# Kernel tuning notes

Hardware: AMD Instinct MI355X
Metric: run time of the kernel (lower is better)

The kernel has to match this reference:

```python
import jax, jax.numpy as jnp
import numpy as np

T, H, I, E, TOP_K = 4096, 2048, 768, 16, 2


def _pack_i2s(tern):
    # tern: int8 in {-1,0,1}, shape [..., K] with K % 4 == 0
    m = (tern + 1).astype(jnp.uint8)  # map to {0,1,2}
    m = m.reshape(*tern.shape[:-1], -1, 4)
    return (m[..., 0] | (m[..., 1] << 2) | (m[..., 2] << 4) | (m[..., 3] << 6)).astype(jnp.uint8)


def _quantize_alpha(alpha):
    # per-column alpha -> int8 with global scale (quantize_alpha_int8)
    scale = jnp.maximum(jnp.abs(alpha).max(), 1e-8) / 127.0
    q = jnp.clip(jnp.round(alpha / scale), -128, 127).astype(jnp.int8)
    return q, scale.astype(jnp.float32)


def _unpack_i2s(packed, K, alpha):
    # packed: uint8 [..., N, K//4]; alpha: [..., K] per input column
    shifts = jnp.array([0, 2, 4, 6], dtype=jnp.uint8)
    ext = (packed[..., None] >> shifts) & jnp.uint8(3)  # [..., N, K//4, 4]
    vals = ext.reshape(*packed.shape[:-1], K).astype(jnp.float32) - 1.0  # {-1,0,1}
    return vals * alpha[..., None, :]


def setup_inputs() -> dict:
    key = jax.random.key(0)
    ks = jax.random.split(key, 6)
    x = jax.random.normal(ks[0], (T, H), dtype=jnp.float32)
    router_logits = jax.random.normal(ks[1], (T, E), dtype=jnp.float32)
    tern13 = jax.random.randint(ks[2], (E, 2 * I, H), -1, 2, dtype=jnp.int8)
    tern2 = jax.random.randint(ks[3], (E, H, I), -1, 2, dtype=jnp.int8)
    a13 = jax.random.uniform(ks[4], (E, H), minval=0.01, maxval=0.05, dtype=jnp.float32)
    a2 = jax.random.uniform(ks[5], (E, I), minval=0.01, maxval=0.05, dtype=jnp.float32)
    w13_alpha_q, w13_alpha_scale = _quantize_alpha(a13)
    w2_alpha_q, w2_alpha_scale = _quantize_alpha(a2)
    return {
        "x": x,
        "router_logits": router_logits,
        "w13_packed": _pack_i2s(tern13),
        "w13_alpha_q": w13_alpha_q,
        "w13_alpha_scale": w13_alpha_scale,
        "w2_packed": _pack_i2s(tern2),
        "w2_alpha_q": w2_alpha_q,
        "w2_alpha_scale": w2_alpha_scale,
    }


def reference(x, router_logits, w13_packed, w13_alpha_q, w13_alpha_scale,
              w2_packed, w2_alpha_q, w2_alpha_scale):
    # dequant int8 alphas, then dequant 2-bit ternary weights
    a13 = w13_alpha_q.astype(jnp.float32) * w13_alpha_scale  # [E, H]
    a2 = w2_alpha_q.astype(jnp.float32) * w2_alpha_scale     # [E, I]
    w13 = _unpack_i2s(w13_packed, H, a13)  # [E, 2I, H]
    w2 = _unpack_i2s(w2_packed, I, a2)     # [E, H, I]

    # top-k routing with renormalized softmax weights
    probs = jax.nn.softmax(router_logits, axis=-1)
    topw, topi = jax.lax.top_k(probs, TOP_K)           # [T, k]
    topw = topw / topw.sum(axis=-1, keepdims=True)
    combine = jnp.sum(jax.nn.one_hot(topi, E, dtype=x.dtype) * topw[..., None], axis=1)  # [T, E]

    # grouped expert matmuls (dense dispatch over experts)
    gu = jnp.einsum('th,enh->ten', x, w13)             # [T, E, 2I]
    gate, up = jnp.split(gu, 2, axis=-1)
    act = jax.nn.silu(gate) * up                       # [T, E, I]
    down = jnp.einsum('tei,ehi->teh', act, w2)         # [T, E, H]
    return jnp.einsum('te,teh->th', combine, down)     # [T, H]
```

## Files before the change

### kernel.cpp

```cpp
#include <hip/hip_runtime.h>
#include <stdint.h>

#define T_TOK 4096
#define HDIM  2048
#define IDIM  768
#define NEXP  16
#define NPAIR (T_TOK * 2)
#define PAIR_CAP_FB (NPAIR + 128)
#define PAIR_CAP    (NPAIR + 256)

typedef float f32x4 __attribute__((ext_vector_type(4)));
typedef __bf16 bf16x8 __attribute__((ext_vector_type(8)));
typedef unsigned short u16x8 __attribute__((ext_vector_type(8)));
typedef unsigned int u32;
typedef const __attribute__((address_space(1))) u32* as1_u32p;
typedef __attribute__((address_space(3))) u32* as3_u32p;

__device__ __forceinline__ unsigned short f2bf(float f) {
  u32 u = __float_as_uint(f);
  u += 0x7FFFu + ((u >> 16) & 1u);
  return (unsigned short)(u >> 16);
}

__device__ __forceinline__ unsigned short tb(int m) {
  return m == 0 ? (unsigned short)0xBF80 : (m == 2 ? (unsigned short)0x3F80 : (unsigned short)0);
}

__device__ __forceinline__ f32x4 mfma16(bf16x8 a, bf16x8 b, f32x4 c) {
  return __builtin_amdgcn_mfma_f32_16x16x32_bf16(a, b, c, 0, 0, 0);
}

__global__ __launch_bounds__(256) void route_kernel(
    const float* __restrict__ logits, int* __restrict__ counts,
    int* __restrict__ t2i, float* __restrict__ t2w) {
  const int t = blockIdx.x * 256 + threadIdx.x;
  if (t >= T_TOK) return;
  const float* l = logits + t * NEXP;
  float m0 = -1e30f, m1 = -1e30f;
  int i0 = 0, i1 = 0;
#pragma unroll
  for (int j = 0; j < NEXP; ++j) {
    const float v = l[j];
    if (v > m0) { m1 = m0; i1 = i0; m0 = v; i0 = j; }
    else if (v > m1) { m1 = v; i1 = j; }
  }
  const float w0 = 1.0f / (1.0f + expf(m1 - m0));
  t2i[t] = i0 | (i1 << 8);
  t2w[t] = w0;
  atomicAdd(&counts[i0], 1);
  atomicAdd(&counts[i1], 1);
}

__global__ void scan_kernel(const int* __restrict__ counts,
                            int* __restrict__ offs, int* __restrict__ cursor) {
  if (threadIdx.x == 0) {
    int s = 0;
    for (int e = 0; e < NEXP; ++e) { offs[e] = s; cursor[e] = s; s += counts[e]; }
    offs[NEXP] = s;
  }
}

__global__ __launch_bounds__(256) void fill_kernel(
    const int* __restrict__ t2i, const float* __restrict__ t2w,
    int* __restrict__ cursor, int* __restrict__ pair_token,
    float* __restrict__ pair_wt, int* __restrict__ pair_eid) {
  const int t = blockIdx.x * 256 + threadIdx.x;
  if (t >= T_TOK) return;
  const int ii = t2i[t];
  const float w0 = t2w[t];
  const int i0 = ii & 255, i1 = (ii >> 8) & 255;
  const int p0 = atomicAdd(&cursor[i0], 1);
  pair_token[p0] = t; pair_wt[p0] = w0; pair_eid[p0] = i0;
  const int p1 = atomicAdd(&cursor[i1], 1);
  pair_token[p1] = t; pair_wt[p1] = 1.0f - w0; pair_eid[p1] = i1;
}

__global__ __launch_bounds__(256) void xg_kernel(
    const float* __restrict__ x, const int* __restrict__ a13q,
    const float* __restrict__ s13p, const int* __restrict__ pair_token,
    const int* __restrict__ pair_eid, unsigned short* __restrict__ xg) {
  const int p = blockIdx.x;
  const int t = pair_token[p];
  const int e = pair_eid[p];
  const float s13 = *s13p;
  const int h0 = threadIdx.x * 8;
  const float* xp = x + (size_t)t * HDIM + h0;
  const int* ap = a13q + (size_t)e * HDIM + h0;
  const float4 x0 = ((const float4*)xp)[0];
  const float4 x1 = ((const float4*)xp)[1];
  const int4 a0 = ((const int4*)ap)[0];
  const int4 a1 = ((const int4*)ap)[1];
  u16x8 q;
  q[0] = f2bf(x0.x * (float)a0.x * s13);
  q[1] = f2bf(x0.y * (float)a0.y * s13);
  q[2] = f2bf(x0.z * (float)a0.z * s13);
  q[3] = f2bf(x0.w * (float)a0.w * s13);
  q[4] = f2bf(x1.x * (float)a1.x * s13);
  q[5] = f2bf(x1.y * (float)a1.y * s13);
  q[6] = f2bf(x1.z * (float)a1.z * s13);
  q[7] = f2bf(x1.w * (float)a1.w * s13);
  *(u16x8*)(xg + (size_t)p * HDIM + h0) = q;
}

__global__ __launch_bounds__(256, 2) void gemm1_kernel(
    const int* __restrict__ w13p, const int* __restrict__ a2q,
    const float* __restrict__ s2p, const int* __restrict__ counts,
    const int* __restrict__ offs, const unsigned short* __restrict__ xg,
    unsigned short* __restrict__ act) {
  const int nT = blockIdx.x;
  const int mT = blockIdx.y;
  const int e  = blockIdx.z;
  const int cnt = counts[e];
  if (mT * 256 >= cnt) return;
  const int base = offs[e];
  const int tid = threadIdx.x;

  __shared__ unsigned short sA[256 * 32];
  __shared__ unsigned short sB[128 * 40];
  __shared__ uint2 lut[256];

  {
    const int b = tid;
    const u32 lo = (u32)tb(b & 3) | ((u32)tb((b >> 2) & 3) << 16);
    const u32 hi = (u32)tb((b >> 4) & 3) | ((u32)tb((b >> 6) & 3) << 16);
    lut[b] = make_uint2(lo, hi);
  }
  __syncthreads();

  const int wave = tid >> 6, lane = tid & 63;
  const int quad = lane >> 4, ln = lane & 15;

  const int bn = tid >> 1, bhalf = tid & 1;
  const int grow = (bn < 64) ? (nT * 64 + bn) : (IDIM + nT * 64 + (bn - 64));
  const int* bptr = w13p + ((size_t)e * (2 * IDIM) + grow) * (HDIM / 4) + bhalf * 4;
  unsigned short* sBw = sB + bn * 40 + (bhalf << 4);

  const int arow = lane >> 2;
  const int acol = (lane & 3) * 8;
  const size_t arow0 = (size_t)(base + mT * 256);

  f32x4 acc[4][8] = {};

  for (int kt = 0; kt < HDIM / 32; ++kt) {
#pragma unroll
    for (int c = 0; c < 4; ++c) {
      const unsigned short* gp =
          xg + (arow0 + c * 64 + wave * 16 + arow) * HDIM + kt * 32 + acol;
      unsigned short* lp = sA + (c * 64 + wave * 16) * 32;
      __builtin_amdgcn_global_load_lds((as1_u32p)(const void*)gp, (as3_u32p)(void*)lp, 16, 0, 0);
    }
    {
      const int4 wv = *(const int4*)(bptr + kt * 8);
      const uint2 q0 = lut[wv.x], q1 = lut[wv.y], q2 = lut[wv.z], q3 = lut[wv.w];
      *(uint2*)(sBw + 0) = q0;
      *(uint2*)(sBw + 4) = q1;
      *(uint2*)(sBw + 8) = q2;
      *(uint2*)(sBw + 12) = q3;
    }
    __syncthreads();
    bf16x8 af[4];
#pragma unroll
    for (int mi = 0; mi < 4; ++mi)
      af[mi] = *(const bf16x8*)(sA + (wave * 64 + mi * 16 + ln) * 32 + quad * 8);
#pragma unroll
    for (int ni = 0; ni < 8; ++ni) {
      const bf16x8 bf = *(const bf16x8*)(sB + (ni * 16 + ln) * 40 + quad * 8);
#pragma unroll
      for (int mi = 0; mi < 4; ++mi) acc[mi][ni] = mfma16(af[mi], bf, acc[mi][ni]);
    }
    __syncthreads();
  }

  const float s2 = *s2p;
#pragma unroll
  for (int ni = 0; ni < 4; ++ni) {
    const int i = nT * 64 + ni * 16 + ln;
    const float a2v = (float)a2q[e * IDIM + i] * s2;
#pragma unroll
    for (int mi = 0; mi < 4; ++mi) {
      const f32x4 g = acc[mi][ni];
      const f32x4 u = acc[mi][ni + 4];
#pragma unroll
      for (int r = 0; r < 4; ++r) {
        const int m = mT * 256 + wave * 64 + mi * 16 + quad * 4 + r;
        if (m < cnt) {
          const float gv = g[r];
          const float av = gv / (1.0f + __expf(-gv)) * u[r];
          act[(size_t)(base + m) * IDIM + i] = f2bf(av * a2v);
        }
      }
    }
  }
}

__global__ __launch_bounds__(256, 2) void gemm2_kernel(
    const int* __restrict__ w2p, const int* __restrict__ counts,
    const int* __restrict__ offs, const int* __restrict__ pair_token,
    const float* __restrict__ pair_wt, const unsigned short* __restrict__ act,
    float* __restrict__ out) {
  const int nT = blockIdx.x;
  const int mT = blockIdx.y;
  const int e  = blockIdx.z;
  const int cnt = counts[e];
  if (mT * 256 >= cnt) return;
  const int base = offs[e];
  const int tid = threadIdx.x;

  __shared__ unsigned short sA[256 * 32];
  __shared__ unsigned short sB[128 * 40];
  __shared__ uint2 lut[256];
  __shared__ int stok[256];
  __shared__ float swt[256];

  {
    const int b = tid;
    const u32 lo = (u32)tb(b & 3) | ((u32)tb((b >> 2) & 3) << 16);
    const u32 hi = (u32)tb((b >> 4) & 3) | ((u32)tb((b >> 6) & 3) << 16);
    lut[b] = make_uint2(lo, hi);
    const int m = mT * 256 + tid;
    const bool v = m < cnt;
    stok[tid] = v ? pair_token[base + m] : 0;
    swt[tid]  = v ? pair_wt[base + m] : 0.0f;
  }
  __syncthreads();

  const int wave = tid >> 6, lane = tid & 63;
  const int quad = lane >> 4, ln = lane & 15;

  const int bn = tid >> 1, bhalf = tid & 1;
  const int* bptr = w2p + ((size_t)e * HDIM + nT * 128 + bn) * (IDIM / 4) + bhalf * 4;
  unsigned short* sBw = sB + bn * 40 + (bhalf << 4);

  const int arow = lane >> 2;
  const int acol = (lane & 3) * 8;
  const size_t arow0 = (size_t)(base + mT * 256);

  f32x4 acc[4][8] = {};

  for (int kt = 0; kt < IDIM / 32; ++kt) {
#pragma unroll
    for (int c = 0; c < 4; ++c) {
      const unsigned short* gp =
          act + (arow0 + c * 64 + wave * 16 + arow) * IDIM + kt * 32 + acol;
      unsigned short* lp = sA + (c * 64 + wave * 16) * 32;
      __builtin_amdgcn_global_load_lds((as1_u32p)(const void*)gp, (as3_u32p)(void*)lp, 16, 0, 0);
    }
    {
      const int4 wv = *(const int4*)(bptr + kt * 8);
      const uint2 q0 = lut[wv.x], q1 = lut[wv.y], q2 = lut[wv.z], q3 = lut[wv.w];
      *(uint2*)(sBw + 0) = q0;
      *(uint2*)(sBw + 4) = q1;
      *(uint2*)(sBw + 8) = q2;
      *(uint2*)(sBw + 12) = q3;
    }
    __syncthreads();
    bf16x8 af[4];
#pragma unroll
    for (int mi = 0; mi < 4; ++mi)
      af[mi] = *(const bf16x8*)(sA + (wave * 64 + mi * 16 + ln) * 32 + quad * 8);
#pragma unroll
    for (int ni = 0; ni < 8; ++ni) {
      const bf16x8 bf = *(const bf16x8*)(sB + (ni * 16 + ln) * 40 + quad * 8);
#pragma unroll
      for (int mi = 0; mi < 4; ++mi) acc[mi][ni] = mfma16(af[mi], bf, acc[mi][ni]);
    }
    __syncthreads();
  }

#pragma unroll
  for (int mi = 0; mi < 4; ++mi) {
#pragma unroll
    for (int r = 0; r < 4; ++r) {
      const int ml = wave * 64 + mi * 16 + quad * 4 + r;
      const int m = mT * 256 + ml;
      if (m < cnt) {
        const float wgt = swt[ml];
        float* orow = out + (size_t)stok[ml] * HDIM + nT * 128;
#pragma unroll
        for (int ni = 0; ni < 8; ++ni)
          atomicAdd(orow + ni * 16 + ln, wgt * acc[mi][ni][r]);
      }
    }
  }
}

__global__ __launch_bounds__(256) void gemm1_fb(
    const float* __restrict__ x, const int* __restrict__ w13p,
    const int* __restrict__ a13q, const float* __restrict__ s13p,
    const int* __restrict__ a2q, const float* __restrict__ s2p,
    const int* __restrict__ counts, const int* __restrict__ offs,
    const int* __restrict__ pair_token, unsigned short* __restrict__ act) {
  const int nT = blockIdx.x;
  const int mT = blockIdx.y;
  const int e  = blockIdx.z;
  const int cnt = counts[e];
  if (mT * 128 >= cnt) return;
  const int base = offs[e];
  const int tid = threadIdx.x;

  __shared__ float ald[HDIM];
  __shared__ unsigned short sA[128 * 40];
  __shared__ unsigned short sB[128 * 40];
  __shared__ int stok[128];

  const float s13 = *s13p;
  for (int h = tid; h < HDIM; h += 256) ald[h] = (float)a13q[e * HDIM + h] * s13;
  if (tid < 128) {
    const int m = mT * 128 + tid;
    stok[tid] = (m < cnt) ? pair_token[base + m] : 0;
  }
  __syncthreads();

  const int wave = tid >> 6, lane = tid & 63;
  const int quad = lane >> 4, ln = lane & 15;

  const int ar = tid >> 1, akh = (tid & 1) << 4;
  const size_t xrow = (size_t)stok[ar] * HDIM;
  const int bn = tid >> 1, bhalf = tid & 1;
  const int grow = (bn < 64) ? (nT * 64 + bn) : (IDIM + nT * 64 + (bn - 64));
  const int* bptr = w13p + ((size_t)e * (2 * IDIM) + grow) * (HDIM / 4) + bhalf * 4;
  unsigned short* sAw = sA + ar * 40 + akh;
  unsigned short* sBw = sB + bn * 40 + (bhalf << 4);

  f32x4 acc[2][8] = {};

  for (int kt = 0; kt < HDIM / 32; ++kt) {
    const int k0 = kt * 32;
    {
      const float* xp = x + xrow + k0 + akh;
      const float* ap = ald + k0 + akh;
      const float4 f0 = ((const float4*)xp)[0];
      const float4 f1 = ((const float4*)xp)[1];
      const float4 f2 = ((const float4*)xp)[2];
      const float4 f3 = ((const float4*)xp)[3];
      u16x8 q0, q1;
      q0[0] = f2bf(f0.x * ap[0]);  q0[1] = f2bf(f0.y * ap[1]);
      q0[2] = f2bf(f0.z * ap[2]);  q0[3] = f2bf(f0.w * ap[3]);
      q0[4] = f2bf(f1.x * ap[4]);  q0[5] = f2bf(f1.y * ap[5]);
      q0[6] = f2bf(f1.z * ap[6]);  q0[7] = f2bf(f1.w * ap[7]);
      q1[0] = f2bf(f2.x * ap[8]);  q1[1] = f2bf(f2.y * ap[9]);
      q1[2] = f2bf(f2.z * ap[10]); q1[3] = f2bf(f2.w * ap[11]);
      q1[4] = f2bf(f3.x * ap[12]); q1[5] = f2bf(f3.y * ap[13]);
      q1[6] = f2bf(f3.z * ap[14]); q1[7] = f2bf(f3.w * ap[15]);
      *(u16x8*)(sAw) = q0;
      *(u16x8*)(sAw + 8) = q1;
    }
    {
      const int4 wv = *(const int4*)(bptr + kt * 8);
      u16x8 q0, q1;
      q0[0] = tb(wv.x & 3); q0[1] = tb((wv.x >> 2) & 3); q0[2] = tb((wv.x >> 4) & 3); q0[3] = tb((wv.x >> 6) & 3);
      q0[4] = tb(wv.y & 3); q0[5] = tb((wv.y >> 2) & 3); q0[6] = tb((wv.y >> 4) & 3); q0[7] = tb((wv.y >> 6) & 3);
      q1[0] = tb(wv.z & 3); q1[1] = tb((wv.z >> 2) & 3); q1[2] = tb((wv.z >> 4) & 3); q1[3] = tb((wv.z >> 6) & 3);
      q1[4] = tb(wv.w & 3); q1[5] = tb((wv.w >> 2) & 3); q1[6] = tb((wv.w >> 4) & 3); q1[7] = tb((wv.w >> 6) & 3);
      *(u16x8*)(sBw) = q0;
      *(u16x8*)(sBw + 8) = q1;
    }
    __syncthreads();
    bf16x8 af[2];
#pragma unroll
    for (int mi = 0; mi < 2; ++mi)
      af[mi] = *(const bf16x8*)(sA + (wave * 32 + mi * 16 + ln) * 40 + quad * 8);
#pragma unroll
    for (int ni = 0; ni < 8; ++ni) {
      const bf16x8 bf = *(const bf16x8*)(sB + (ni * 16 + ln) * 40 + quad * 8);
      acc[0][ni] = mfma16(af[0], bf, acc[0][ni]);
      acc[1][ni] = mfma16(af[1], bf, acc[1][ni]);
    }
    __syncthreads();
  }

  const float s2 = *s2p;
#pragma unroll
  for (int ni = 0; ni < 4; ++ni) {
    const int i = nT * 64 + ni * 16 + ln;
    const float a2v = (float)a2q[e * IDIM + i] * s2;
#pragma unroll
    for (int mi = 0; mi < 2; ++mi) {
      const f32x4 g = acc[mi][ni];
      const f32x4 u = acc[mi][ni + 4];
#pragma unroll
      for (int r = 0; r < 4; ++r) {
        const int m = mT * 128 + wave * 32 + mi * 16 + quad * 4 + r;
        if (m < cnt) {
          const float gv = g[r];
          const float av = gv / (1.0f + __expf(-gv)) * u[r];
          act[(size_t)(base + m) * IDIM + i] = f2bf(av * a2v);
        }
      }
    }
  }
}

__global__ __launch_bounds__(256) void gemm2_fb(
    const int* __restrict__ w2p, const int* __restrict__ counts,
    const int* __restrict__ offs, const int* __restrict__ pair_token,
    const float* __restrict__ pair_wt, const unsigned short* __restrict__ act,
    float* __restrict__ out) {
  const int nT = blockIdx.x;
  const int mT = blockIdx.y;
  const int e  = blockIdx.z;
  const int cnt = counts[e];
  if (mT * 128 >= cnt) return;
  const int base = offs[e];
  const int tid = threadIdx.x;

  __shared__ unsigned short sA[128 * 32];
  __shared__ unsigned short sB[128 * 40];
  __shared__ int stok[128];
  __shared__ float swt[128];

  if (tid < 128) {
    const int m = mT * 128 + tid;
    const bool v = m < cnt;
    stok[tid] = v ? pair_token[base + m] : 0;
    swt[tid]  = v ? pair_wt[base + m] : 0.0f;
  }

  const int wave = tid >> 6, lane = tid & 63;
  const int quad = lane >> 4, ln = lane & 15;

  const int bn = tid >> 1, bhalf = tid & 1;
  const int* bptr = w2p + ((size_t)e * HDIM + nT * 128 + bn) * (IDIM / 4) + bhalf * 4;
  unsigned short* sBw = sB + bn * 40 + (bhalf << 4);

  const int arow = lane >> 2;
  const int acol8 = (lane & 3) * 8;
  const size_t arow0 = (size_t)(base + mT * 128);

  f32x4 acc[2][8] = {};

  for (int kt = 0; kt < IDIM / 32; ++kt) {
#pragma unroll
    for (int c = 0; c < 2; ++c) {
      const int r = c * 64 + wave * 16 + arow;
      const unsigned short* gp = act + (arow0 + r) * IDIM + kt * 32 + acol8;
      unsigned short* lp = sA + (c * 64 + wave * 16) * 32;
      __builtin_amdgcn_global_load_lds((as1_u32p)(const void*)gp, (as3_u32p)(void*)lp, 16, 0, 0);
    }
    {
      const int4 wv = *(const int4*)(bptr + kt * 8);
      u16x8 q0, q1;
      q0[0] = tb(wv.x & 3); q0[1] = tb((wv.x >> 2) & 3); q0[2] = tb((wv.x >> 4) & 3); q0[3] = tb((wv.x >> 6) & 3);
      q0[4] = tb(wv.y & 3); q0[5] = tb((wv.y >> 2) & 3); q0[6] = tb((wv.y >> 4) & 3); q0[7] = tb((wv.y >> 6) & 3);
      q1[0] = tb(wv.z & 3); q1[1] = tb((wv.z >> 2) & 3); q1[2] = tb((wv.z >> 4) & 3); q1[3] = tb((wv.z >> 6) & 3);
      q1[4] = tb(wv.w & 3); q1[5] = tb((wv.w >> 2) & 3); q1[6] = tb((wv.w >> 4) & 3); q1[7] = tb((wv.w >> 6) & 3);
      *(u16x8*)(sBw) = q0;
      *(u16x8*)(sBw + 8) = q1;
    }
    __syncthreads();
    bf16x8 af[2];
#pragma unroll
    for (int mi = 0; mi < 2; ++mi)
      af[mi] = *(const bf16x8*)(sA + (wave * 32 + mi * 16 + ln) * 32 + quad * 8);
#pragma unroll
    for (int ni = 0; ni < 8; ++ni) {
      const bf16x8 bf = *(const bf16x8*)(sB + (ni * 16 + ln) * 40 + quad * 8);
      acc[0][ni] = mfma16(af[0], bf, acc[0][ni]);
      acc[1][ni] = mfma16(af[1], bf, acc[1][ni]);
    }
    __syncthreads();
  }

#pragma unroll
  for (int mi = 0; mi < 2; ++mi) {
#pragma unroll
    for (int r = 0; r < 4; ++r) {
      const int ml = wave * 32 + mi * 16 + quad * 4 + r;
      const int m = mT * 128 + ml;
      if (m < cnt) {
        const float wgt = swt[ml];
        float* orow = out + (size_t)stok[ml] * HDIM + nT * 128;
#pragma unroll
        for (int ni = 0; ni < 8; ++ni)
          atomicAdd(orow + ni * 16 + ln, wgt * acc[mi][ni][r]);
      }
    }
  }
}

extern "C" void kernel_launch(void* const* d_in, const int* in_sizes, int n_in,
                              void* d_out, int out_size, void* d_ws, size_t ws_size,
                              hipStream_t stream) {
  const float* x      = (const float*)d_in[0];
  const float* logits = (const float*)d_in[1];
  const int*   w13p   = (const int*)d_in[2];
  const int*   a13q   = (const int*)d_in[3];
  const float* s13    = (const float*)d_in[4];
  const int*   w2p    = (const int*)d_in[5];
  const int*   a2q    = (const int*)d_in[6];
  const float* s2     = (const float*)d_in[7];
  float* out = (float*)d_out;

  char* ws = (char*)d_ws;
  int*   counts     = (int*)(ws + 0);
  int*   cursor     = (int*)(ws + 64);
  int*   offs       = (int*)(ws + 128);
  int*   t2i        = (int*)(ws + 256);
  float* t2w        = (float*)(ws + 256 + 4 * T_TOK);
  int*   pair_token = (int*)(ws + 256 + 8 * T_TOK);
  float* pair_wt    = (float*)(ws + 256 + 8 * T_TOK + 4 * PAIR_CAP);
  int*   pair_eid   = (int*)(ws + 256 + 8 * T_TOK + 8 * PAIR_CAP);
  const size_t hdr_end = ((size_t)(256 + 8 * T_TOK + 12 * PAIR_CAP) + 255) & ~(size_t)255;

  const size_t xg_bytes  = (size_t)PAIR_CAP * HDIM * 2;
  const size_t act_bytes = (size_t)PAIR_CAP * IDIM * 2;
  const size_t need_new = hdr_end + xg_bytes + act_bytes;

  hipMemsetAsync(counts, 0, 256, stream);
  hipMemsetAsync(out, 0, (size_t)out_size * sizeof(float), stream);

  route_kernel<<<T_TOK / 256, 256, 0, stream>>>(logits, counts, t2i, t2w);
  scan_kernel<<<1, 64, 0, stream>>>(counts, offs, cursor);
  fill_kernel<<<T_TOK / 256, 256, 0, stream>>>(t2i, t2w, cursor, pair_token, pair_wt, pair_eid);

  if (ws_size >= need_new) {
    unsigned short* xg  = (unsigned short*)(ws + hdr_end);
    unsigned short* act = (unsigned short*)(ws + hdr_end + xg_bytes);
    xg_kernel<<<NPAIR, 256, 0, stream>>>(x, a13q, s13, pair_token, pair_eid, xg);
    gemm1_kernel<<<dim3(12, 16, 16), 256, 0, stream>>>(w13p, a2q, s2, counts, offs, xg, act);
    gemm2_kernel<<<dim3(16, 16, 16), 256, 0, stream>>>(w2p, counts, offs, pair_token,
                                                       pair_wt, act, out);
  } else {
    unsigned short* act = (unsigned short*)(ws + hdr_end);
    gemm1_fb<<<dim3(12, 32, 16), 256, 0, stream>>>(x, w13p, a13q, s13, a2q, s2,
                                                   counts, offs, pair_token, act);
    gemm2_fb<<<dim3(16, 32, 16), 256, 0, stream>>>(w2p, counts, offs, pair_token,
                                                   pair_wt, act, out);
  }
}
```

Measured before the change: 395.3 us.

## Repack ternary weights compactly, shrink GEMM M-tile, replace atomics with combine kernel

Packed ternary weights are stored one byte per int32, so a repack kernel runs each call and compresses them into dense u32 words, cutting the weight bytes the GEMMs read by four. The main GEMMs switch to 128-row M tiles at higher occupancy. gemm2 now writes per-pair outputs to a scratch buffer and a separate combine kernel does the weighted top-2 sum, removing float atomics and the output memset. The cost is extra repack passes on every call, a large fp32 scratch buffer and more kernel launches.

```diff
diff --git a/kernel.cpp b/kernel.cpp
--- a/kernel.cpp
+++ b/kernel.cpp
@@ -6,8 +6,7 @@
 #define IDIM  768
 #define NEXP  16
 #define NPAIR (T_TOK * 2)
-#define PAIR_CAP_FB (NPAIR + 128)
-#define PAIR_CAP    (NPAIR + 256)
+#define PAIR_CAP (NPAIR + 256)
 
 typedef float f32x4 __attribute__((ext_vector_type(4)));
 typedef __bf16 bf16x8 __attribute__((ext_vector_type(8)));
@@ -63,7 +62,8 @@
 __global__ __launch_bounds__(256) void fill_kernel(
     const int* __restrict__ t2i, const float* __restrict__ t2w,
     int* __restrict__ cursor, int* __restrict__ pair_token,
-    float* __restrict__ pair_wt, int* __restrict__ pair_eid) {
+    float* __restrict__ pair_wt, int* __restrict__ pair_eid,
+    int* __restrict__ t2p0, int* __restrict__ t2p1) {
   const int t = blockIdx.x * 256 + threadIdx.x;
   if (t >= T_TOK) return;
   const int ii = t2i[t];
@@ -73,6 +73,21 @@
   pair_token[p0] = t; pair_wt[p0] = w0; pair_eid[p0] = i0;
   const int p1 = atomicAdd(&cursor[i1], 1);
   pair_token[p1] = t; pair_wt[p1] = 1.0f - w0; pair_eid[p1] = i1;
+  t2p0[t] = p0; t2p1[t] = p1;
+}
+
+__global__ __launch_bounds__(256) void repack_kernel(
+    const int* __restrict__ w, u32* __restrict__ o) {
+  const int j0 = (blockIdx.x * 256 + threadIdx.x) * 4;
+  const int4* w4 = (const int4*)w;
+  uint4 r;
+#pragma unroll
+  for (int k = 0; k < 4; ++k) {
+    const int4 a = w4[j0 + k];
+    ((u32*)&r)[k] = (u32)(a.x & 255) | ((u32)(a.y & 255) << 8) |
+                    ((u32)(a.z & 255) << 16) | ((u32)(a.w & 255) << 24);
+  }
+  ((uint4*)o)[blockIdx.x * 256 + threadIdx.x] = r;
 }
 
 __global__ __launch_bounds__(256) void xg_kernel(
@@ -102,8 +117,8 @@
   *(u16x8*)(xg + (size_t)p * HDIM + h0) = q;
 }
 
-__global__ __launch_bounds__(256, 2) void gemm1_kernel(
-    const int* __restrict__ w13p, const int* __restrict__ a2q,
+__global__ __launch_bounds__(256, 3) void gemm1_kernel(
+    const u32* __restrict__ wq13, const int* __restrict__ a2q,
     const float* __restrict__ s2p, const int* __restrict__ counts,
     const int* __restrict__ offs, const unsigned short* __restrict__ xg,
     unsigned short* __restrict__ act) {
@@ -111,11 +126,11 @@
   const int mT = blockIdx.y;
   const int e  = blockIdx.z;
   const int cnt = counts[e];
-  if (mT * 256 >= cnt) return;
+  if (mT * 128 >= cnt) return;
   const int base = offs[e];
   const int tid = threadIdx.x;
 
-  __shared__ unsigned short sA[256 * 32];
+  __shared__ unsigned short sA[128 * 32];
   __shared__ unsigned short sB[128 * 40];
   __shared__ uint2 lut[256];
 
@@ -132,15 +147,218 @@
 
   const int bn = tid >> 1, bhalf = tid & 1;
   const int grow = (bn < 64) ? (nT * 64 + bn) : (IDIM + nT * 64 + (bn - 64));
+  const u32* bptr = wq13 + ((size_t)e * (2 * IDIM) + grow) * (HDIM / 16) + bhalf;
+  unsigned short* sBw = sB + bn * 40 + (bhalf << 4);
+
+  const int arow = lane >> 2;
+  const int acol = (lane & 3) * 8;
+  const size_t arow0 = (size_t)(base + mT * 128);
+
+  f32x4 acc[2][8] = {};
+
+  for (int kt = 0; kt < HDIM / 32; ++kt) {
+#pragma unroll
+    for (int c = 0; c < 2; ++c) {
+      const unsigned short* gp =
+          xg + (arow0 + c * 64 + wave * 16 + arow) * HDIM + kt * 32 + acol;
+      unsigned short* lp = sA + (c * 64 + wave * 16) * 32;
+      __builtin_amdgcn_global_load_lds((as1_u32p)(const void*)gp, (as3_u32p)(void*)lp, 16, 0, 0);
+    }
+    {
+      const u32 wb = bptr[kt * 2];
+      const uint2 q0 = lut[wb & 255], q1 = lut[(wb >> 8) & 255];
+      const uint2 q2 = lut[(wb >> 16) & 255], q3 = lut[wb >> 24];
+      *(uint2*)(sBw + 0) = q0;
+      *(uint2*)(sBw + 4) = q1;
+      *(uint2*)(sBw + 8) = q2;
+      *(uint2*)(sBw + 12) = q3;
+    }
+    __syncthreads();
+    bf16x8 af[2];
+#pragma unroll
+    for (int mi = 0; mi < 2; ++mi)
+      af[mi] = *(const bf16x8*)(sA + (wave * 32 + mi * 16 + ln) * 32 + quad * 8);
+#pragma unroll
+    for (int ni = 0; ni < 8; ++ni) {
+      const bf16x8 bf = *(const bf16x8*)(sB + (ni * 16 + ln) * 40 + quad * 8);
+      acc[0][ni] = mfma16(af[0], bf, acc[0][ni]);
+      acc[1][ni] = mfma16(af[1], bf, acc[1][ni]);
+    }
+    __syncthreads();
+  }
+
+  const float s2 = *s2p;
+#pragma unroll
+  for (int ni = 0; ni < 4; ++ni) {
+    const int i = nT * 64 + ni * 16 + ln;
+    const float a2v = (float)a2q[e * IDIM + i] * s2;
+#pragma unroll
+    for (int mi = 0; mi < 2; ++mi) {
+      const f32x4 g = acc[mi][ni];
+      const f32x4 u = acc[mi][ni + 4];
+#pragma unroll
+      for (int r = 0; r < 4; ++r) {
+        const int m = mT * 128 + wave * 32 + mi * 16 + quad * 4 + r;
+        if (m < cnt) {
+          const float gv = g[r];
+          const float av = gv / (1.0f + __expf(-gv)) * u[r];
+          act[(size_t)(base + m) * IDIM + i] = f2bf(av * a2v);
+        }
+      }
+    }
+  }
+}
+
+template <bool ATOMIC>
+__global__ __launch_bounds__(256, 3) void gemm2_kernel(
+    const u32* __restrict__ wq2, const int* __restrict__ counts,
+    const int* __restrict__ offs, const int* __restrict__ pair_token,
+    const float* __restrict__ pair_wt, const unsigned short* __restrict__ act,
+    float* __restrict__ dst) {
+  const int nT = blockIdx.x;
+  const int mT = blockIdx.y;
+  const int e  = blockIdx.z;
+  const int cnt = counts[e];
+  if (mT * 128 >= cnt) return;
+  const int base = offs[e];
+  const int tid = threadIdx.x;
+
+  __shared__ unsigned short sA[128 * 32];
+  __shared__ unsigned short sB[128 * 40];
+  __shared__ uint2 lut[256];
+  __shared__ int stok[128];
+  __shared__ float swt[128];
+
+  {
+    const int b = tid;
+    const u32 lo = (u32)tb(b & 3) | ((u32)tb((b >> 2) & 3) << 16);
+    const u32 hi = (u32)tb((b >> 4) & 3) | ((u32)tb((b >> 6) & 3) << 16);
+    lut[b] = make_uint2(lo, hi);
+    if (ATOMIC && tid < 128) {
+      const int m = mT * 128 + tid;
+      const bool v = m < cnt;
+      stok[tid] = v ? pair_token[base + m] : 0;
+      swt[tid]  = v ? pair_wt[base + m] : 0.0f;
+    }
+  }
+  __syncthreads();
+
+  const int wave = tid >> 6, lane = tid & 63;
+  const int quad = lane >> 4, ln = lane & 15;
+
+  const int bn = tid >> 1, bhalf = tid & 1;
+  const u32* bptr = wq2 + ((size_t)e * HDIM + nT * 128 + bn) * (IDIM / 16) + bhalf;
+  unsigned short* sBw = sB + bn * 40 + (bhalf << 4);
+
+  const int arow = lane >> 2;
+  const int acol = (lane & 3) * 8;
+  const size_t arow0 = (size_t)(base + mT * 128);
+
+  f32x4 acc[2][8] = {};
+
+  for (int kt = 0; kt < IDIM / 32; ++kt) {
+#pragma unroll
+    for (int c = 0; c < 2; ++c) {
+      const unsigned short* gp =
+          act + (arow0 + c * 64 + wave * 16 + arow) * IDIM + kt * 32 + acol;
+      unsigned short* lp = sA + (c * 64 + wave * 16) * 32;
+      __builtin_amdgcn_global_load_lds((as1_u32p)(const void*)gp, (as3_u32p)(void*)lp, 16, 0, 0);
+    }
+    {
+      const u32 wb = bptr[kt * 2];
+      const uint2 q0 = lut[wb & 255], q1 = lut[(wb >> 8) & 255];
+      const uint2 q2 = lut[(wb >> 16) & 255], q3 = lut[wb >> 24];
+      *(uint2*)(sBw + 0) = q0;
+      *(uint2*)(sBw + 4) = q1;
+      *(uint2*)(sBw + 8) = q2;
+      *(uint2*)(sBw + 12) = q3;
+    }
+    __syncthreads();
+    bf16x8 af[2];
+#pragma unroll
+    for (int mi = 0; mi < 2; ++mi)
+      af[mi] = *(const bf16x8*)(sA + (wave * 32 + mi * 16 + ln) * 32 + quad * 8);
+#pragma unroll
+    for (int ni = 0; ni < 8; ++ni) {
+      const bf16x8 bf = *(const bf16x8*)(sB + (ni * 16 + ln) * 40 + quad * 8);
+      acc[0][ni] = mfma16(af[0], bf, acc[0][ni]);
+      acc[1][ni] = mfma16(af[1], bf, acc[1][ni]);
+    }
+    __syncthreads();
+  }
+
+#pragma unroll
+  for (int mi = 0; mi < 2; ++mi) {
+#pragma unroll
+    for (int r = 0; r < 4; ++r) {
+      const int ml = wave * 32 + mi * 16 + quad * 4 + r;
+      const int m = mT * 128 + ml;
+      if (m < cnt) {
+        if (ATOMIC) {
+          const float wgt = swt[ml];
+          float* orow = dst + (size_t)stok[ml] * HDIM + nT * 128;
+#pragma unroll
+          for (int ni = 0; ni < 8; ++ni)
+            atomicAdd(orow + ni * 16 + ln, wgt * acc[mi][ni][r]);
+        } else {
+          float* drow = dst + (size_t)(base + m) * HDIM + nT * 128;
+#pragma unroll
+          for (int ni = 0; ni < 8; ++ni)
+            drow[ni * 16 + ln] = acc[mi][ni][r];
+        }
+      }
+    }
+  }
+}
+
+__global__ __launch_bounds__(256) void combine_kernel(
+    const int* __restrict__ t2p0, const int* __restrict__ t2p1,
+    const float* __restrict__ t2w, const float* __restrict__ down,
+    float* __restrict__ out) {
+  const int t = blockIdx.x;
+  const float w0 = t2w[t];
+  const float w1 = 1.0f - w0;
+  const float* d0 = down + (size_t)t2p0[t] * HDIM;
+  const float* d1 = down + (size_t)t2p1[t] * HDIM;
+  float* o = out + (size_t)t * HDIM;
+  const int h = threadIdx.x * 8;
+  const f32x4 a0 = *(const f32x4*)(d0 + h);
+  const f32x4 a1 = *(const f32x4*)(d0 + h + 4);
+  const f32x4 b0 = *(const f32x4*)(d1 + h);
+  const f32x4 b1 = *(const f32x4*)(d1 + h + 4);
+  *(f32x4*)(o + h) = w0 * a0 + w1 * b0;
+  *(f32x4*)(o + h + 4) = w0 * a1 + w1 * b1;
+}
+
+__global__ __launch_bounds__(256, 2) void gemm1_c(
+    const int* __restrict__ w13p, const int* __restrict__ a2q,
+    const float* __restrict__ s2p, const int* __restrict__ counts,
+    const int* __restrict__ offs, const unsigned short* __restrict__ xg,
+    unsigned short* __restrict__ act) {
+  const int nT = blockIdx.x, mT = blockIdx.y, e = blockIdx.z;
+  const int cnt = counts[e];
+  if (mT * 256 >= cnt) return;
+  const int base = offs[e];
+  const int tid = threadIdx.x;
+  __shared__ unsigned short sA[256 * 32];
+  __shared__ unsigned short sB[128 * 40];
+  __shared__ uint2 lut[256];
+  {
+    const int b = tid;
+    const u32 lo = (u32)tb(b & 3) | ((u32)tb((b >> 2) & 3) << 16);
+    const u32 hi = (u32)tb((b >> 4) & 3) | ((u32)tb((b >> 6) & 3) << 16);
+    lut[b] = make_uint2(lo, hi);
+  }
+  __syncthreads();
+  const int wave = tid >> 6, lane = tid & 63;
+  const int quad = lane >> 4, ln = lane & 15;
+  const int bn = tid >> 1, bhalf = tid & 1;
+  const int grow = (bn < 64) ? (nT * 64 + bn) : (IDIM + nT * 64 + (bn - 64));
   const int* bptr = w13p + ((size_t)e * (2 * IDIM) + grow) * (HDIM / 4) + bhalf * 4;
   unsigned short* sBw = sB + bn * 40 + (bhalf << 4);
-
-  const int arow = lane >> 2;
-  const int acol = (lane & 3) * 8;
+  const int arow = lane >> 2, acol = (lane & 3) * 8;
   const size_t arow0 = (size_t)(base + mT * 256);
-
   f32x4 acc[4][8] = {};
-
   for (int kt = 0; kt < HDIM / 32; ++kt) {
 #pragma unroll
     for (int c = 0; c < 4; ++c) {
@@ -152,10 +370,8 @@
     {
       const int4 wv = *(const int4*)(bptr + kt * 8);
       const uint2 q0 = lut[wv.x], q1 = lut[wv.y], q2 = lut[wv.z], q3 = lut[wv.w];
-      *(uint2*)(sBw + 0) = q0;
-      *(uint2*)(sBw + 4) = q1;
-      *(uint2*)(sBw + 8) = q2;
-      *(uint2*)(sBw + 12) = q3;
+      *(uint2*)(sBw + 0) = q0; *(uint2*)(sBw + 4) = q1;
+      *(uint2*)(sBw + 8) = q2; *(uint2*)(sBw + 12) = q3;
     }
     __syncthreads();
     bf16x8 af[4];
@@ -170,7 +386,6 @@
     }
     __syncthreads();
   }
-
   const float s2 = *s2p;
 #pragma unroll
   for (int ni = 0; ni < 4; ++ni) {
@@ -193,25 +408,21 @@
   }
 }
 
-__global__ __launch_bounds__(256, 2) void gemm2_kernel(
+__global__ __launch_bounds__(256, 2) void gemm2_c(
     const int* __restrict__ w2p, const int* __restrict__ counts,
     const int* __restrict__ offs, const int* __restrict__ pair_token,
     const float* __restrict__ pair_wt, const unsigned short* __restrict__ act,
     float* __restrict__ out) {
-  const int nT = blockIdx.x;
-  const int mT = blockIdx.y;
-  const int e  = blockIdx.z;
+  const int nT = blockIdx.x, mT = blockIdx.y, e = blockIdx.z;
   const int cnt = counts[e];
   if (mT * 256 >= cnt) return;
   const int base = offs[e];
   const int tid = threadIdx.x;
-
   __shared__ unsigned short sA[256 * 32];
   __shared__ unsigned short sB[128 * 40];
   __shared__ uint2 lut[256];
   __shared__ int stok[256];
   __shared__ float swt[256];
-
   {
     const int b = tid;
     const u32 lo = (u32)tb(b & 3) | ((u32)tb((b >> 2) & 3) << 16);
@@ -223,20 +434,14 @@
     swt[tid]  = v ? pair_wt[base + m] : 0.0f;
   }
   __syncthreads();
-
   const int wave = tid >> 6, lane = tid & 63;
   const int quad = lane >> 4, ln = lane & 15;
-
   const int bn = tid >> 1, bhalf = tid & 1;
   const int* bptr = w2p + ((size_t)e * HDIM + nT * 128 + bn) * (IDIM / 4) + bhalf * 4;
   unsigned short* sBw = sB + bn * 40 + (bhalf << 4);
-
-  const int arow = lane >> 2;
-  const int acol = (lane & 3) * 8;
+  const int arow = lane >> 2, acol = (lane & 3) * 8;
   const size_t arow0 = (size_t)(base + mT * 256);
-
   f32x4 acc[4][8] = {};
-
   for (int kt = 0; kt < IDIM / 32; ++kt) {
 #pragma unroll
     for (int c = 0; c < 4; ++c) {
@@ -248,10 +453,8 @@
     {
       const int4 wv = *(const int4*)(bptr + kt * 8);
       const uint2 q0 = lut[wv.x], q1 = lut[wv.y], q2 = lut[wv.z], q3 = lut[wv.w];
-      *(uint2*)(sBw + 0) = q0;
-      *(uint2*)(sBw + 4) = q1;
-      *(uint2*)(sBw + 8) = q2;
-      *(uint2*)(sBw + 12) = q3;
+      *(uint2*)(sBw + 0) = q0; *(uint2*)(sBw + 4) = q1;
+      *(uint2*)(sBw + 8) = q2; *(uint2*)(sBw + 12) = q3;
     }
     __syncthreads();
     bf16x8 af[4];
@@ -266,207 +469,12 @@
     }
     __syncthreads();
   }
-
 #pragma unroll
   for (int mi = 0; mi < 4; ++mi) {
 #pragma unroll
     for (int r = 0; r < 4; ++r) {
       const int ml = wave * 64 + mi * 16 + quad * 4 + r;
       const int m = mT * 256 + ml;
-      if (m < cnt) {
-        const float wgt = swt[ml];
-        float* orow = out + (size_t)stok[ml] * HDIM + nT * 128;
-#pragma unroll
-        for (int ni = 0; ni < 8; ++ni)
-          atomicAdd(orow + ni * 16 + ln, wgt * acc[mi][ni][r]);
-      }
-    }
-  }
-}
-
-__global__ __launch_bounds__(256) void gemm1_fb(
-    const float* __restrict__ x, const int* __restrict__ w13p,
-    const int* __restrict__ a13q, const float* __restrict__ s13p,
-    const int* __restrict__ a2q, const float* __restrict__ s2p,
-    const int* __restrict__ counts, const int* __restrict__ offs,
-    const int* __restrict__ pair_token, unsigned short* __restrict__ act) {
-  const int nT = blockIdx.x;
-  const int mT = blockIdx.y;
-  const int e  = blockIdx.z;
-  const int cnt = counts[e];
-  if (mT * 128 >= cnt) return;
-  const int base = offs[e];
-  const int tid = threadIdx.x;
-
-  __shared__ float ald[HDIM];
-  __shared__ unsigned short sA[128 * 40];
-  __shared__ unsigned short sB[128 * 40];
-  __shared__ int stok[128];
-
-  const float s13 = *s13p;
-  for (int h = tid; h < HDIM; h += 256) ald[h] = (float)a13q[e * HDIM + h] * s13;
-  if (tid < 128) {
-    const int m = mT * 128 + tid;
-    stok[tid] = (m < cnt) ? pair_token[base + m] : 0;
-  }
-  __syncthreads();
-
-  const int wave = tid >> 6, lane = tid & 63;
-  const int quad = lane >> 4, ln = lane & 15;
-
-  const int ar = tid >> 1, akh = (tid & 1) << 4;
-  const size_t xrow = (size_t)stok[ar] * HDIM;
-  const int bn = tid >> 1, bhalf = tid & 1;
-  const int grow = (bn < 64) ? (nT * 64 + bn) : (IDIM + nT * 64 + (bn - 64));
-  const int* bptr = w13p + ((size_t)e * (2 * IDIM) + grow) * (HDIM / 4) + bhalf * 4;
-  unsigned short* sAw = sA + ar * 40 + akh;
-  unsigned short* sBw = sB + bn * 40 + (bhalf << 4);
-
-  f32x4 acc[2][8] = {};
-
-  for (int kt = 0; kt < HDIM / 32; ++kt) {
-    const int k0 = kt * 32;
-    {
-      const float* xp = x + xrow + k0 + akh;
-      const float* ap = ald + k0 + akh;
-      const float4 f0 = ((const float4*)xp)[0];
-      const float4 f1 = ((const float4*)xp)[1];
-      const float4 f2 = ((const float4*)xp)[2];
-      const float4 f3 = ((const float4*)xp)[3];
-      u16x8 q0, q1;
-      q0[0] = f2bf(f0.x * ap[0]);  q0[1] = f2bf(f0.y * ap[1]);
-      q0[2] = f2bf(f0.z * ap[2]);  q0[3] = f2bf(f0.w * ap[3]);
-      q0[4] = f2bf(f1.x * ap[4]);  q0[5] = f2bf(f1.y * ap[5]);
-      q0[6] = f2bf(f1.z * ap[6]);  q0[7] = f2bf(f1.w * ap[7]);
-      q1[0] = f2bf(f2.x * ap[8]);  q1[1] = f2bf(f2.y * ap[9]);
-      q1[2] = f2bf(f2.z * ap[10]); q1[3] = f2bf(f2.w * ap[11]);
-      q1[4] = f2bf(f3.x * ap[12]); q1[5] = f2bf(f3.y * ap[13]);
-      q1[6] = f2bf(f3.z * ap[14]); q1[7] = f2bf(f3.w * ap[15]);
-      *(u16x8*)(sAw) = q0;
-      *(u16x8*)(sAw + 8) = q1;
-    }
-    {
-      const int4 wv = *(const int4*)(bptr + kt * 8);
-      u16x8 q0, q1;
-      q0[0] = tb(wv.x & 3); q0[1] = tb((wv.x >> 2) & 3); q0[2] = tb((wv.x >> 4) & 3); q0[3] = tb((wv.x >> 6) & 3);
-      q0[4] = tb(wv.y & 3); q0[5] = tb((wv.y >> 2) & 3); q0[6] = tb((wv.y >> 4) & 3); q0[7] = tb((wv.y >> 6) & 3);
-      q1[0] = tb(wv.z & 3); q1[1] = tb((wv.z >> 2) & 3); q1[2] = tb((wv.z >> 4) & 3); q1[3] = tb((wv.z >> 6) & 3);
-      q1[4] = tb(wv.w & 3); q1[5] = tb((wv.w >> 2) & 3); q1[6] = tb((wv.w >> 4) & 3); q1[7] = tb((wv.w >> 6) & 3);
-      *(u16x8*)(sBw) = q0;
-      *(u16x8*)(sBw + 8) = q1;
-    }
-    __syncthreads();
-    bf16x8 af[2];
-#pragma unroll
-    for (int mi = 0; mi < 2; ++mi)
-      af[mi] = *(const bf16x8*)(sA + (wave * 32 + mi * 16 + ln) * 40 + quad * 8);
-#pragma unroll
-    for (int ni = 0; ni < 8; ++ni) {
-      const bf16x8 bf = *(const bf16x8*)(sB + (ni * 16 + ln) * 40 + quad * 8);
-      acc[0][ni] = mfma16(af[0], bf, acc[0][ni]);
-      acc[1][ni] = mfma16(af[1], bf, acc[1][ni]);
-    }
-    __syncthreads();
-  }
-
-  const float s2 = *s2p;
-#pragma unroll
-  for (int ni = 0; ni < 4; ++ni) {
-    const int i = nT * 64 + ni * 16 + ln;
-    const float a2v = (float)a2q[e * IDIM + i] * s2;
-#pragma unroll
-    for (int mi = 0; mi < 2; ++mi) {
-      const f32x4 g = acc[mi][ni];
-      const f32x4 u = acc[mi][ni + 4];
-#pragma unroll
-      for (int r = 0; r < 4; ++r) {
-        const int m = mT * 128 + wave * 32 + mi * 16 + quad * 4 + r;
-        if (m < cnt) {
-          const float gv = g[r];
-          const float av = gv / (1.0f + __expf(-gv)) * u[r];
-          act[(size_t)(base + m) * IDIM + i] = f2bf(av * a2v);
-        }
-      }
-    }
-  }
-}
-
-__global__ __launch_bounds__(256) void gemm2_fb(
-    const int* __restrict__ w2p, const int* __restrict__ counts,
-    const int* __restrict__ offs, const int* __restrict__ pair_token,
-    const float* __restrict__ pair_wt, const unsigned short* __restrict__ act,
-    float* __restrict__ out) {
-  const int nT = blockIdx.x;
-  const int mT = blockIdx.y;
-  const int e  = blockIdx.z;
-  const int cnt = counts[e];
-  if (mT * 128 >= cnt) return;
-  const int base = offs[e];
-  const int tid = threadIdx.x;
-
-  __shared__ unsigned short sA[128 * 32];
-  __shared__ unsigned short sB[128 * 40];
-  __shared__ int stok[128];
-  __shared__ float swt[128];
-
-  if (tid < 128) {
-    const int m = mT * 128 + tid;
-    const bool v = m < cnt;
-    stok[tid] = v ? pair_token[base + m] : 0;
-    swt[tid]  = v ? pair_wt[base + m] : 0.0f;
-  }
-
-  const int wave = tid >> 6, lane = tid & 63;
-  const int quad = lane >> 4, ln = lane & 15;
-
-  const int bn = tid >> 1, bhalf = tid & 1;
-  const int* bptr = w2p + ((size_t)e * HDIM + nT * 128 + bn) * (IDIM / 4) + bhalf * 4;
-  unsigned short* sBw = sB + bn * 40 + (bhalf << 4);
-
-  const int arow = lane >> 2;
-  const int acol8 = (lane & 3) * 8;
-  const size_t arow0 = (size_t)(base + mT * 128);
-
-  f32x4 acc[2][8] = {};
-
-  for (int kt = 0; kt < IDIM / 32; ++kt) {
-#pragma unroll
-    for (int c = 0; c < 2; ++c) {
-      const int r = c * 64 + wave * 16 + arow;
-      const unsigned short* gp = act + (arow0 + r) * IDIM + kt * 32 + acol8;
-      unsigned short* lp = sA + (c * 64 + wave * 16) * 32;
-      __builtin_amdgcn_global_load_lds((as1_u32p)(const void*)gp, (as3_u32p)(void*)lp, 16, 0, 0);
-    }
-    {
-      const int4 wv = *(const int4*)(bptr + kt * 8);
-      u16x8 q0, q1;
-      q0[0] = tb(wv.x & 3); q0[1] = tb((wv.x >> 2) & 3); q0[2] = tb((wv.x >> 4) & 3); q0[3] = tb((wv.x >> 6) & 3);
-      q0[4] = tb(wv.y & 3); q0[5] = tb((wv.y >> 2) & 3); q0[6] = tb((wv.y >> 4) & 3); q0[7] = tb((wv.y >> 6) & 3);
-      q1[0] = tb(wv.z & 3); q1[1] = tb((wv.z >> 2) & 3); q1[2] = tb((wv.z >> 4) & 3); q1[3] = tb((wv.z >> 6) & 3);
-      q1[4] = tb(wv.w & 3); q1[5] = tb((wv.w >> 2) & 3); q1[6] = tb((wv.w >> 4) & 3); q1[7] = tb((wv.w >> 6) & 3);
-      *(u16x8*)(sBw) = q0;
-      *(u16x8*)(sBw + 8) = q1;
-    }
-    __syncthreads();
-    bf16x8 af[2];
-#pragma unroll
-    for (int mi = 0; mi < 2; ++mi)
-      af[mi] = *(const bf16x8*)(sA + (wave * 32 + mi * 16 + ln) * 32 + quad * 8);
-#pragma unroll
-    for (int ni = 0; ni < 8; ++ni) {
-      const bf16x8 bf = *(const bf16x8*)(sB + (ni * 16 + ln) * 40 + quad * 8);
-      acc[0][ni] = mfma16(af[0], bf, acc[0][ni]);
-      acc[1][ni] = mfma16(af[1], bf, acc[1][ni]);
-    }
-    __syncthreads();
-  }
-
-#pragma unroll
-  for (int mi = 0; mi < 2; ++mi) {
-#pragma unroll
-    for (int r = 0; r < 4; ++r) {
-      const int ml = wave * 32 + mi * 16 + quad * 4 + r;
-      const int m = mT * 128 + ml;
       if (m < cnt) {
         const float wgt = swt[ml];
         float* orow = out + (size_t)stok[ml] * HDIM + nT * 128;
@@ -497,34 +505,55 @@
   int*   offs       = (int*)(ws + 128);
   int*   t2i        = (int*)(ws + 256);
   float* t2w        = (float*)(ws + 256 + 4 * T_TOK);
-  int*   pair_token = (int*)(ws + 256 + 8 * T_TOK);
-  float* pair_wt    = (float*)(ws + 256 + 8 * T_TOK + 4 * PAIR_CAP);
-  int*   pair_eid   = (int*)(ws + 256 + 8 * T_TOK + 8 * PAIR_CAP);
-  const size_t hdr_end = ((size_t)(256 + 8 * T_TOK + 12 * PAIR_CAP) + 255) & ~(size_t)255;
-
-  const size_t xg_bytes  = (size_t)PAIR_CAP * HDIM * 2;
-  const size_t act_bytes = (size_t)PAIR_CAP * IDIM * 2;
-  const size_t need_new = hdr_end + xg_bytes + act_bytes;
+  int*   t2p0       = (int*)(ws + 256 + 8 * T_TOK);
+  int*   t2p1       = (int*)(ws + 256 + 12 * T_TOK);
+  int*   pair_token = (int*)(ws + 256 + 16 * T_TOK);
+  float* pair_wt    = (float*)(ws + 256 + 16 * T_TOK + 4 * PAIR_CAP);
+  int*   pair_eid   = (int*)(ws + 256 + 16 * T_TOK + 8 * PAIR_CAP);
+  const size_t hdr_end = ((size_t)(256 + 16 * T_TOK + 12 * PAIR_CAP) + 255) & ~(size_t)255;
+
+  const size_t n32_13 = (size_t)NEXP * 2 * IDIM * (HDIM / 16);
+  const size_t n32_2  = (size_t)NEXP * HDIM * (IDIM / 16);
+  const size_t rp13_b = n32_13 * 4, rp2_b = n32_2 * 4;
+  const size_t xg_b   = (size_t)PAIR_CAP * HDIM * 2;
+  const size_t act_b  = (size_t)PAIR_CAP * IDIM * 2;
+  const size_t down_b = (size_t)PAIR_CAP * HDIM * 4;
+
+  const size_t need_A = hdr_end + rp13_b + rp2_b + xg_b + act_b + down_b;
+  const size_t need_B = hdr_end + rp13_b + rp2_b + xg_b + act_b;
 
   hipMemsetAsync(counts, 0, 256, stream);
-  hipMemsetAsync(out, 0, (size_t)out_size * sizeof(float), stream);
-
   route_kernel<<<T_TOK / 256, 256, 0, stream>>>(logits, counts, t2i, t2w);
   scan_kernel<<<1, 64, 0, stream>>>(counts, offs, cursor);
-  fill_kernel<<<T_TOK / 256, 256, 0, stream>>>(t2i, t2w, cursor, pair_token, pair_wt, pair_eid);
-
-  if (ws_size >= need_new) {
+  fill_kernel<<<T_TOK / 256, 256, 0, stream>>>(t2i, t2w, cursor, pair_token, pair_wt,
+                                               pair_eid, t2p0, t2p1);
+
+  if (ws_size >= need_B) {
+    u32* rp13 = (u32*)(ws + hdr_end);
+    u32* rp2  = (u32*)(ws + hdr_end + rp13_b);
+    unsigned short* xg  = (unsigned short*)(ws + hdr_end + rp13_b + rp2_b);
+    unsigned short* act = (unsigned short*)(ws + hdr_end + rp13_b + rp2_b + xg_b);
+    repack_kernel<<<(int)(n32_13 / 1024), 256, 0, stream>>>(w13p, rp13);
+    repack_kernel<<<(int)(n32_2 / 1024), 256, 0, stream>>>(w2p, rp2);
+    xg_kernel<<<NPAIR, 256, 0, stream>>>(x, a13q, s13, pair_token, pair_eid, xg);
+    gemm1_kernel<<<dim3(12, 32, 16), 256, 0, stream>>>(rp13, a2q, s2, counts, offs, xg, act);
+    if (ws_size >= need_A) {
+      float* down = (float*)(ws + need_B);
+      gemm2_kernel<false><<<dim3(16, 32, 16), 256, 0, stream>>>(
+          rp2, counts, offs, pair_token, pair_wt, act, down);
+      combine_kernel<<<T_TOK, 256, 0, stream>>>(t2p0, t2p1, t2w, down, out);
+    } else {
+      hipMemsetAsync(out, 0, (size_t)out_size * sizeof(float), stream);
+      gemm2_kernel<true><<<dim3(16, 32, 16), 256, 0, stream>>>(
+          rp2, counts, offs, pair_token, pair_wt, act, out);
+    }
+  } else {
     unsigned short* xg  = (unsigned short*)(ws + hdr_end);
-    unsigned short* act = (unsigned short*)(ws + hdr_end + xg_bytes);
+    unsigned short* act = (unsigned short*)(ws + hdr_end + xg_b);
+    hipMemsetAsync(out, 0, (size_t)out_size * sizeof(float), stream);
     xg_kernel<<<NPAIR, 256, 0, stream>>>(x, a13q, s13, pair_token, pair_eid, xg);
-    gemm1_kernel<<<dim3(12, 16, 16), 256, 0, stream>>>(w13p, a2q, s2, counts, offs, xg, act);
-    gemm2_kernel<<<dim3(16, 16, 16), 256, 0, stream>>>(w2p, counts, offs, pair_token,
-                                                       pair_wt, act, out);
-  } else {
-    unsigned short* act = (unsigned short*)(ws + hdr_end);
-    gemm1_fb<<<dim3(12, 32, 16), 256, 0, stream>>>(x, w13p, a13q, s13, a2q, s2,
-                                                   counts, offs, pair_token, act);
-    gemm2_fb<<<dim3(16, 32, 16), 256, 0, stream>>>(w2p, counts, offs, pair_token,
-                                                   pair_wt, act, out);
-  }
-}
+    gemm1_c<<<dim3(12, 16, 16), 256, 0, stream>>>(w13p, a2q, s2, counts, offs, xg, act);
+    gemm2_c<<<dim3(16, 16, 16), 256, 0, stream>>>(w2p, counts, offs, pair_token,
+                                                  pair_wt, act, out);
+  }
+}
```

New measurement: 390.6 us. Within noise of the previous version (-1.2%).
